# Performance work log

Hardware: AMD Instinct MI355X
Metric: run time of the kernel (lower is better)

The kernel has to match this reference:

```python
import jax, jax.numpy as jnp
import numpy as np

ROPE_BASE = 10000.0

def rope_2d(x, h, w):
    # x: (b, h, w, c); 2D RoPE, first half of pair-channels rotated by row angle, second by col angle
    b, _, _, c = x.shape
    k_max = c // 4  # c // (2 * num_spatial_dims)
    theta = 1.0 / (ROPE_BASE ** (jnp.arange(k_max, dtype=jnp.float32) / k_max))  # (k_max,)
    ang_h = jnp.arange(h, dtype=jnp.float32)[:, None] * theta  # (h, k_max)
    ang_w = jnp.arange(w, dtype=jnp.float32)[:, None] * theta  # (w, k_max)
    # angles: (h, w, 2*k_max) = cat([i*theta, j*theta], -1)
    angles = jnp.concatenate([
        jnp.broadcast_to(ang_h[:, None, :], (h, w, k_max)),
        jnp.broadcast_to(ang_w[None, :, :], (h, w, k_max)),
    ], axis=-1)
    cos = jnp.cos(angles)  # (h, w, c//2)
    sin = jnp.sin(angles)
    xr = x[..., 0::2]  # consecutive-pair real parts (b,h,w,c//2)
    xi = x[..., 1::2]
    out_r = xr * cos - xi * sin
    out_i = xr * sin + xi * cos
    return jnp.stack([out_r, out_i], axis=-1).reshape(b, h, w, c)

def linear_attention_fwd(x, h, w, qk_w, qk_b, lepe_w, lepe_b, num_heads=4):
    b, n, c = x.shape
    head_dim = c // num_heads
    qk = x @ qk_w.T + qk_b  # (b, n, 2c)
    q, k = qk[..., :c], qk[..., c:]
    v = x
    q = jax.nn.elu(q) + 1.0
    k = jax.nn.elu(k) + 1.0
    q_rope = rope_2d(q.reshape(b, h, w, c), h, w).reshape(b, n, num_heads, head_dim).transpose(0, 2, 1, 3)
    k_rope = rope_2d(k.reshape(b, h, w, c), h, w).reshape(b, n, num_heads, head_dim).transpose(0, 2, 1, 3)
    qh = q.reshape(b, n, num_heads, head_dim).transpose(0, 2, 1, 3)  # (b,H,n,d)
    kh = k.reshape(b, n, num_heads, head_dim).transpose(0, 2, 1, 3)
    vh = v.reshape(b, n, num_heads, head_dim).transpose(0, 2, 1, 3)
    k_mean = kh.mean(axis=2)  # (b,H,d)
    z = 1.0 / (jnp.einsum('bhnd,bhd->bhn', qh, k_mean) + 1e-6)  # (b,H,n)
    inv_n = 1.0 / n
    kv = jnp.einsum('bhnd,bhne->bhde', k_rope, vh) * inv_n  # (b,H,d,d)
    out = jnp.einsum('bhnd,bhde->bhne', q_rope, kv) * z[..., None]  # (b,H,n,d)
    out = out.transpose(0, 2, 1, 3).reshape(b, n, c)
    # LePE: depthwise 3x3 conv on v in NCHW
    v_img = v.reshape(b, h, w, c).transpose(0, 3, 1, 2)  # (b,c,h,w)
    lepe = jax.lax.conv_general_dilated(
        v_img, lepe_w, window_strides=(1, 1), padding='SAME',
        feature_group_count=c, dimension_numbers=('NCHW', 'OIHW', 'NCHW'))
    lepe = lepe + lepe_b[None, :, None, None]
    out = out + lepe.transpose(0, 2, 3, 1).reshape(b, n, c)
    return out.transpose(0, 2, 1).reshape(b, c, h, w)

def setup_inputs() -> dict:
    key = jax.random.key(0)
    ks = jax.random.split(key, 5)
    b, h, w, c = 16, 128, 128, 64
    n = h * w
    x = jax.random.normal(ks[0], (b, n, c), dtype=jnp.float32)
    qk_w = jax.random.normal(ks[1], (2 * c, c), dtype=jnp.float32) * (1.0 / np.sqrt(c))
    qk_b = jax.random.normal(ks[2], (2 * c,), dtype=jnp.float32) * 0.02
    lepe_w = jax.random.normal(ks[3], (c, 1, 3, 3), dtype=jnp.float32) * (1.0 / 3.0)
    lepe_b = jax.random.normal(ks[4], (c,), dtype=jnp.float32) * 0.02
    return {"x": x, "h": h, "w": w, "qk_w": qk_w, "qk_b": qk_b, "lepe_w": lepe_w, "lepe_b": lepe_b}

def reference(x, h, w, qk_w, qk_b, lepe_w, lepe_b):
    return linear_attention_fwd(x, h, w, qk_w, qk_b, lepe_w, lepe_b, num_heads=4)
```

## Files before the change

kernel.cpp:

```cpp
#include <hip/hip_runtime.h>

#define B_   16
#define C_   64
#define HH   128
#define WW   128
#define NN   (HH*WW)
#define NH   4
#define HD   16
#define PADB 72
#define PADO 66

typedef short short8 __attribute__((ext_vector_type(8)));
typedef short short4v __attribute__((ext_vector_type(4)));
typedef float f32x4  __attribute__((ext_vector_type(4)));

__device__ __forceinline__ float act_elu1(float v) {
    return v > 0.f ? v + 1.f : __expf(v);
}
__device__ __forceinline__ short f2bf(float f) {
    union { float f; unsigned u; } v; v.f = f;
    unsigned r = (v.u + 0x7FFFu + ((v.u >> 16) & 1u)) >> 16;
    return (short)r;
}

#define NEG_L2_10K_OVER16 (-0.8304820237218406f)

__global__ __launch_bounds__(256) void la_phase1(
    const float* __restrict__ x, const float* __restrict__ qk_w,
    const float* __restrict__ qk_b, float* __restrict__ g_part)
{
    __shared__ __align__(16) char pool[4*64*PADB*2 + 256*4];
    short* sW  = (short*)pool;
    short* sX  = sW  + 64*PADB;
    short* sXT = sX  + 64*PADB;
    short* sKT = sXT + 64*PADB;
    float* kmp = (float*)(sKT + 64*PADB);

    const int tid  = threadIdx.x;
    const int w    = tid >> 6;
    const int ln   = tid & 15;
    const int quad = (tid >> 4) & 3;
    const int b    = blockIdx.y;
    const int nblk = blockIdx.x;
    const float* xb = x + (size_t)b * (size_t)(NN * C_);

    #pragma unroll
    for (int it = 0; it < 4; ++it) {
        int idx = tid + 256*it;
        int row = idx & 63, k4 = (idx >> 6) << 2;
        float4 wv = *(const float4*)(qk_w + (64 + row)*64 + k4);
        short4v s4 = { f2bf(wv.x), f2bf(wv.y), f2bf(wv.z), f2bf(wv.w) };
        *(short4v*)(sW + row*PADB + k4) = s4;
    }

    float bias[4];
    #pragma unroll
    for (int nt = 0; nt < 4; ++nt) bias[nt] = qk_b[64 + 16*nt + ln];

    f32x4 acc2 = {0.f, 0.f, 0.f, 0.f};
    float kmacc[4] = {0.f, 0.f, 0.f, 0.f};

    for (int ck = 0; ck < 4; ++ck) {
        const int n0 = nblk*256 + ck*64;
        if (ck) __syncthreads();
        #pragma unroll
        for (int it = 0; it < 4; ++it) {
            int idx = tid + 256*it;
            int row = idx & 63, k4 = (idx >> 6) << 2;
            float4 xv = *(const float4*)(xb + (size_t)(n0 + row)*C_ + k4);
            short4v s4 = { f2bf(xv.x), f2bf(xv.y), f2bf(xv.z), f2bf(xv.w) };
            *(short4v*)(sX + row*PADB + k4) = s4;
            sXT[(k4+0)*PADB + row] = s4.x;
            sXT[(k4+1)*PADB + row] = s4.y;
            sXT[(k4+2)*PADB + row] = s4.z;
            sXT[(k4+3)*PADB + row] = s4.w;
        }
        __syncthreads();

        f32x4 acc[4];
        #pragma unroll
        for (int nt = 0; nt < 4; ++nt) acc[nt] = (f32x4){0.f,0.f,0.f,0.f};
        #pragma unroll
        for (int ks = 0; ks < 2; ++ks) {
            short8 a = *(const short8*)(sX + (16*w + ln)*PADB + 32*ks + 8*quad);
            #pragma unroll
            for (int nt = 0; nt < 4; ++nt) {
                short8 bf = *(const short8*)(sW + (16*nt + ln)*PADB + 32*ks + 8*quad);
                acc[nt] = __builtin_amdgcn_mfma_f32_16x16x32_bf16(a, bf, acc[nt], 0, 0, 0);
            }
        }

        #pragma unroll
        for (int nt = 0; nt < 4; ++nt) {
            const int j = 16*nt + ln;
            const int t = j >> 1;
            const float theta = exp2f(NEG_L2_10K_OVER16 * (float)(t & 15));
            const bool isY = (t < 16);
            const float sgn = (j & 1) ? 1.f : -1.f;
            #pragma unroll
            for (int r = 0; r < 4; ++r) {
                float kval = act_elu1(acc[nt][r] + bias[nt]);
                kmacc[nt] += kval;
                float P = __shfl_xor(kval, 1);
                int p_loc = 16*w + 4*quad + r;
                int n = n0 + p_loc;
                float coord = isY ? (float)(n >> 7) : (float)(n & 127);
                float s, c;
                __sincosf(coord * theta, &s, &c);
                float kr = kval*c + sgn*P*s;
                sKT[j*PADB + p_loc] = f2bf(kr);
            }
        }
        __syncthreads();

        #pragma unroll
        for (int ks = 0; ks < 2; ++ks) {
            short8 a  = *(const short8*)(sKT + (16*w + ln)*PADB + 32*ks + 8*quad);
            short8 bf = *(const short8*)(sXT + (16*w + ln)*PADB + 32*ks + 8*quad);
            acc2 = __builtin_amdgcn_mfma_f32_16x16x32_bf16(a, bf, acc2, 0, 0, 0);
        }
    }

    float* pb = g_part + (size_t)(b*64 + nblk) * 1088;
    #pragma unroll
    for (int r = 0; r < 4; ++r)
        pb[w*256 + (4*quad + r)*16 + ln] = acc2[r];

    #pragma unroll
    for (int nt = 0; nt < 4; ++nt) {
        float v = kmacc[nt];
        v += __shfl_xor(v, 16);
        v += __shfl_xor(v, 32);
        if ((tid & 63) < 16) kmp[w*64 + 16*nt + ln] = v;
    }
    __syncthreads();
    if (tid < 64)
        pb[1024 + tid] = kmp[tid] + kmp[64 + tid] + kmp[128 + tid] + kmp[192 + tid];
}

__global__ __launch_bounds__(256) void la_reduce(
    const float* __restrict__ g_part, float* __restrict__ g_kv,
    float* __restrict__ g_km)
{
    int o = blockIdx.x * 256 + threadIdx.x;
    int b = o / 1088;
    int i = o - b * 1088;
    const float* p = g_part + (size_t)(b*64) * 1088 + i;
    float s = 0.f;
    #pragma unroll 8
    for (int nb = 0; nb < 64; ++nb) s += p[(size_t)nb * 1088];
    if (i < 1024) g_kv[b*1024 + i] = s;
    else          g_km[b*64 + (i - 1024)] = s;
}

__global__ __launch_bounds__(256) void la_phase2(
    const float* __restrict__ x, const float* __restrict__ qk_w,
    const float* __restrict__ qk_b, const float* __restrict__ lepe_w,
    const float* __restrict__ lepe_b, const float* __restrict__ g_kv,
    const float* __restrict__ g_km, float* __restrict__ out)
{
    __shared__ __align__(16) char pool[32768];
    short* sX   = (short*)pool;
    short* sW   = sX + 64*PADB;
    float* sOut = (float*)pool;
    short* sQ   = (short*)(pool + 18432);
    short* sKVB = sQ + 64*PADB;

    const int tid  = threadIdx.x;
    const int w    = tid >> 6;
    const int ln   = tid & 15;
    const int quad = (tid >> 4) & 3;
    const int b    = blockIdx.y;
    const int n0   = blockIdx.x * 64;
    const float* xb = x + (size_t)b * (size_t)(NN * C_);
    const float inv_n = 1.f / (float)NN;

    #pragma unroll
    for (int it = 0; it < 4; ++it) {
        int idx = tid + 256*it;
        int row = idx & 63, k4 = (idx >> 6) << 2;
        float4 xv = *(const float4*)(xb + (size_t)(n0 + row)*C_ + k4);
        short4v s4 = { f2bf(xv.x), f2bf(xv.y), f2bf(xv.z), f2bf(xv.w) };
        *(short4v*)(sX + row*PADB + k4) = s4;
        float4 wv = *(const float4*)(qk_w + row*64 + k4);
        short4v s5 = { f2bf(wv.x), f2bf(wv.y), f2bf(wv.z), f2bf(wv.w) };
        *(short4v*)(sW + row*PADB + k4) = s5;
    }
    for (int idx = tid; idx < 1024; idx += 256) {
        int h = idx >> 8, d = (idx >> 4) & 15, e = idx & 15;
        float v = g_kv[b*1024 + idx] * inv_n;
        int rowb = h*16 + e;
        int kpos  = (h & 1) ? 16 + d : d;
        int kzero = (h & 1) ? d : 16 + d;
        sKVB[rowb*40 + kpos]  = f2bf(v);
        sKVB[rowb*40 + kzero] = 0;
    }
    float biasq[4], kmv[4];
    #pragma unroll
    for (int nt = 0; nt < 4; ++nt) {
        biasq[nt] = qk_b[16*nt + ln];
        kmv[nt]   = g_km[b*64 + 16*nt + ln];
    }
    __syncthreads();

    f32x4 acc[4];
    #pragma unroll
    for (int nt = 0; nt < 4; ++nt) acc[nt] = (f32x4){0.f,0.f,0.f,0.f};
    #pragma unroll
    for (int ks = 0; ks < 2; ++ks) {
        short8 a = *(const short8*)(sX + (16*w + ln)*PADB + 32*ks + 8*quad);
        #pragma unroll
        for (int nt = 0; nt < 4; ++nt) {
            short8 bf = *(const short8*)(sW + (16*nt + ln)*PADB + 32*ks + 8*quad);
            acc[nt] = __builtin_amdgcn_mfma_f32_16x16x32_bf16(a, bf, acc[nt], 0, 0, 0);
        }
    }

    float z_all[4][4];
    #pragma unroll
    for (int nt = 0; nt < 4; ++nt) {
        const int j = 16*nt + ln;
        const int t = j >> 1;
        const float theta = exp2f(NEG_L2_10K_OVER16 * (float)(t & 15));
        const bool isY = (t < 16);
        const float sgn = (j & 1) ? 1.f : -1.f;
        #pragma unroll
        for (int r = 0; r < 4; ++r) {
            float qval = act_elu1(acc[nt][r] + biasq[nt]);
            float dotp = qval * kmv[nt];
            dotp += __shfl_xor(dotp, 1);
            dotp += __shfl_xor(dotp, 2);
            dotp += __shfl_xor(dotp, 4);
            dotp += __shfl_xor(dotp, 8);
            z_all[nt][r] = 1.f / (dotp * inv_n + 1e-6f);
            float P = __shfl_xor(qval, 1);
            int p_loc = 16*w + 4*quad + r;
            int n = n0 + p_loc;
            float coord = isY ? (float)(n >> 7) : (float)(n & 127);
            float s, c;
            __sincosf(coord * theta, &s, &c);
            float qr = qval*c + sgn*P*s;
            sQ[p_loc*PADB + j] = f2bf(qr);
        }
    }
    __syncthreads();

    f32x4 accq[4];
    #pragma unroll
    for (int h = 0; h < 4; ++h) accq[h] = (f32x4){0.f,0.f,0.f,0.f};
    #pragma unroll
    for (int P2 = 0; P2 < 2; ++P2) {
        short8 a = *(const short8*)(sQ + (16*w + ln)*PADB + 32*P2 + 8*quad);
        #pragma unroll
        for (int hh = 0; hh < 2; ++hh) {
            int h = 2*P2 + hh;
            short8 bf = *(const short8*)(sKVB + (h*16 + ln)*40 + 8*quad);
            accq[h] = __builtin_amdgcn_mfma_f32_16x16x32_bf16(a, bf, accq[h], 0, 0, 0);
        }
    }
    #pragma unroll
    for (int h = 0; h < 4; ++h)
        #pragma unroll
        for (int r = 0; r < 4; ++r)
            sOut[(16*h + ln)*PADO + 16*w + 4*quad + r] = accq[h][r] * z_all[h][r];
    __syncthreads();

    const int ch = tid >> 2, sub = tid & 3, p0 = 16*sub;
    const int yy = n0 >> 7, xbase = n0 & 127, gx0 = xbase + p0;
    float wv9[9];
    #pragma unroll
    for (int tap = 0; tap < 9; ++tap) wv9[tap] = lepe_w[ch*9 + tap];
    const float lb = lepe_b[ch];
    float accl[16];
    #pragma unroll
    for (int j = 0; j < 16; ++j) accl[j] = 0.f;
    #pragma unroll
    for (int dy = -1; dy <= 1; ++dy) {
        int y2 = yy + dy;
        if ((unsigned)y2 >= HH) continue;
        const float* rp = xb + (size_t)(y2*WW)*C_ + ch;
        float cb[18];
        #pragma unroll
        for (int jj = 0; jj < 18; ++jj) {
            int col = gx0 - 1 + jj;
            cb[jj] = ((unsigned)col < WW) ? rp[(size_t)col*C_] : 0.f;
        }
        float w0 = wv9[(dy+1)*3 + 0], w1 = wv9[(dy+1)*3 + 1], w2 = wv9[(dy+1)*3 + 2];
        #pragma unroll
        for (int j = 0; j < 16; ++j)
            accl[j] += cb[j]*w0 + cb[j+1]*w1 + cb[j+2]*w2;
    }
    float* outp = out + (size_t)b*(size_t)(C_*NN) + (size_t)ch*NN + n0 + p0;
    #pragma unroll
    for (int g = 0; g < 4; ++g) {
        float2 a0 = *(const float2*)(sOut + ch*PADO + p0 + 4*g);
        float2 a1 = *(const float2*)(sOut + ch*PADO + p0 + 4*g + 2);
        float4 o4 = { a0.x + accl[4*g+0] + lb, a0.y + accl[4*g+1] + lb,
                      a1.x + accl[4*g+2] + lb, a1.y + accl[4*g+3] + lb };
        *(float4*)(outp + 4*g) = o4;
    }
}

extern "C" void kernel_launch(void* const* d_in, const int* in_sizes, int n_in,
                              void* d_out, int out_size, void* d_ws, size_t ws_size,
                              hipStream_t stream) {
    const float* x      = (const float*)d_in[0];
    const float* qk_w   = (const float*)d_in[3];
    const float* qk_b   = (const float*)d_in[4];
    const float* lepe_w = (const float*)d_in[5];
    const float* lepe_b = (const float*)d_in[6];
    float* out = (float*)d_out;

    float* g_part = (float*)d_ws;
    float* g_kv   = g_part + 1024*1088;
    float* g_km   = g_kv + 16*1024;

    hipLaunchKernelGGL(la_phase1, dim3(64, B_), dim3(256), 0, stream,
                       x, qk_w, qk_b, g_part);
    hipLaunchKernelGGL(la_reduce, dim3(68), dim3(256), 0, stream,
                       g_part, g_kv, g_km);
    hipLaunchKernelGGL(la_phase2, dim3(256, B_), dim3(256), 0, stream,
                       x, qk_w, qk_b, lepe_w, lepe_b, g_kv, g_km, out);
}
```

Measured before the change: 199.3 us.

## Compute Q in phase1, store bf16 Q, precompute RoPE tables and vectorize LePE

Phase1 now computes both the K and Q projections from the same x tile, writing elu(Q)+1 to a bf16 workspace buffer. Phase2 then reads this buffer directly and no longer reloads x for a second GEMM. A new init kernel precomputes the bf16 weights, a sin/cos RoPE table and transposed LePE weights, which removes per-element sincos work. The A operands are loaded straight from global memory into registers, and the depthwise conv is vectorized across 4 channels with float4 loads. In exchange it adds a 2MB-per-batch bf16 Q write and read round trip plus an extra kernel launch.

```diff
diff --git a/kernel.cpp b/kernel.cpp
--- a/kernel.cpp
+++ b/kernel.cpp
@@ -6,13 +6,13 @@
 #define WW   128
 #define NN   (HH*WW)
 #define NH   4
-#define HD   16
 #define PADB 72
 #define PADO 66
 
 typedef short short8 __attribute__((ext_vector_type(8)));
-typedef short short4v __attribute__((ext_vector_type(4)));
 typedef float f32x4  __attribute__((ext_vector_type(4)));
+
+#define NEG_L2_10K_OVER16 (-0.8304820237218406f)
 
 __device__ __forceinline__ float act_elu1(float v) {
     return v > 0.f ? v + 1.f : __expf(v);
@@ -22,19 +22,46 @@
     unsigned r = (v.u + 0x7FFFu + ((v.u >> 16) & 1u)) >> 16;
     return (short)r;
 }
-
-#define NEG_L2_10K_OVER16 (-0.8304820237218406f)
+__device__ __forceinline__ float bf2f(short s) {
+    union { unsigned u; float f; } v; v.u = ((unsigned)(unsigned short)s) << 16;
+    return v.f;
+}
+__device__ __forceinline__ unsigned cvt2bf(float lo, float hi) {
+    unsigned r;
+    asm("v_cvt_pk_bf16_f32 %0, %1, %2" : "=v"(r) : "v"(lo), "v"(hi));
+    return r;
+}
+
+__global__ __launch_bounds__(256) void la_init(
+    const float* __restrict__ qk_w, const float* __restrict__ lepe_w,
+    float2* __restrict__ g_tab, float* __restrict__ g_wT,
+    short* __restrict__ g_wbf)
+{
+    int i = blockIdx.x * 256 + threadIdx.x;
+    g_wbf[i] = f2bf(qk_w[i]);
+    if (i < 2048) {
+        int coord = i >> 4, t = i & 15;
+        float theta = exp2f(NEG_L2_10K_OVER16 * (float)t);
+        float s, c;
+        __sincosf((float)coord * theta, &s, &c);
+        g_tab[i] = make_float2(c, s);
+    }
+    if (i < 576) {
+        int tap = i >> 6, ch = i & 63;
+        g_wT[i] = lepe_w[ch * 9 + tap];
+    }
+}
 
 __global__ __launch_bounds__(256) void la_phase1(
-    const float* __restrict__ x, const float* __restrict__ qk_w,
-    const float* __restrict__ qk_b, float* __restrict__ g_part)
+    const float* __restrict__ x, const float* __restrict__ qk_b,
+    const short* __restrict__ g_wbf, const float2* __restrict__ g_tab,
+    float* __restrict__ g_part, short* __restrict__ g_q)
 {
-    __shared__ __align__(16) char pool[4*64*PADB*2 + 256*4];
-    short* sW  = (short*)pool;
-    short* sX  = sW  + 64*PADB;
-    short* sXT = sX  + 64*PADB;
+    __shared__ __align__(16) char pool[3*64*PADB*2 + 256*4];
+    short* sXT = (short*)pool;
     short* sKT = sXT + 64*PADB;
-    float* kmp = (float*)(sKT + 64*PADB);
+    short* sQ  = sKT + 64*PADB;
+    float* kmp = (float*)(sQ + 64*PADB);
 
     const int tid  = threadIdx.x;
     const int w    = tid >> 6;
@@ -44,18 +71,12 @@
     const int nblk = blockIdx.x;
     const float* xb = x + (size_t)b * (size_t)(NN * C_);
 
-    #pragma unroll
-    for (int it = 0; it < 4; ++it) {
-        int idx = tid + 256*it;
-        int row = idx & 63, k4 = (idx >> 6) << 2;
-        float4 wv = *(const float4*)(qk_w + (64 + row)*64 + k4);
-        short4v s4 = { f2bf(wv.x), f2bf(wv.y), f2bf(wv.z), f2bf(wv.w) };
-        *(short4v*)(sW + row*PADB + k4) = s4;
-    }
-
-    float bias[4];
-    #pragma unroll
-    for (int nt = 0; nt < 4; ++nt) bias[nt] = qk_b[64 + 16*nt + ln];
+    float biasK[4], biasQ[4];
+    #pragma unroll
+    for (int nt = 0; nt < 4; ++nt) {
+        biasK[nt] = qk_b[64 + 16*nt + ln];
+        biasQ[nt] = qk_b[16*nt + ln];
+    }
 
     f32x4 acc2 = {0.f, 0.f, 0.f, 0.f};
     float kmacc[4] = {0.f, 0.f, 0.f, 0.f};
@@ -68,56 +89,73 @@
             int idx = tid + 256*it;
             int row = idx & 63, k4 = (idx >> 6) << 2;
             float4 xv = *(const float4*)(xb + (size_t)(n0 + row)*C_ + k4);
-            short4v s4 = { f2bf(xv.x), f2bf(xv.y), f2bf(xv.z), f2bf(xv.w) };
-            *(short4v*)(sX + row*PADB + k4) = s4;
-            sXT[(k4+0)*PADB + row] = s4.x;
-            sXT[(k4+1)*PADB + row] = s4.y;
-            sXT[(k4+2)*PADB + row] = s4.z;
-            sXT[(k4+3)*PADB + row] = s4.w;
-        }
-        __syncthreads();
-
-        f32x4 acc[4];
-        #pragma unroll
-        for (int nt = 0; nt < 4; ++nt) acc[nt] = (f32x4){0.f,0.f,0.f,0.f};
+            unsigned p01 = cvt2bf(xv.x, xv.y), p23 = cvt2bf(xv.z, xv.w);
+            sXT[(k4+0)*PADB + row] = (short)p01;
+            sXT[(k4+1)*PADB + row] = (short)(p01 >> 16);
+            sXT[(k4+2)*PADB + row] = (short)p23;
+            sXT[(k4+3)*PADB + row] = (short)(p23 >> 16);
+        }
+        short8 aF[2];
         #pragma unroll
         for (int ks = 0; ks < 2; ++ks) {
-            short8 a = *(const short8*)(sX + (16*w + ln)*PADB + 32*ks + 8*quad);
+            const float* ap = xb + (size_t)(n0 + 16*w + ln)*C_ + 32*ks + 8*quad;
+            float4 a0 = *(const float4*)ap;
+            float4 a1 = *(const float4*)(ap + 4);
+            union { unsigned u[4]; short8 s; } af;
+            af.u[0] = cvt2bf(a0.x, a0.y);
+            af.u[1] = cvt2bf(a0.z, a0.w);
+            af.u[2] = cvt2bf(a1.x, a1.y);
+            af.u[3] = cvt2bf(a1.z, a1.w);
+            aF[ks] = af.s;
+        }
+        f32x4 ak[4], aq[4];
+        #pragma unroll
+        for (int nt = 0; nt < 4; ++nt) { ak[nt] = (f32x4){0.f,0.f,0.f,0.f}; aq[nt] = (f32x4){0.f,0.f,0.f,0.f}; }
+        #pragma unroll
+        for (int ks = 0; ks < 2; ++ks) {
             #pragma unroll
             for (int nt = 0; nt < 4; ++nt) {
-                short8 bf = *(const short8*)(sW + (16*nt + ln)*PADB + 32*ks + 8*quad);
-                acc[nt] = __builtin_amdgcn_mfma_f32_16x16x32_bf16(a, bf, acc[nt], 0, 0, 0);
+                short8 bk = *(const short8*)(g_wbf + (64 + 16*nt + ln)*C_ + 32*ks + 8*quad);
+                short8 bq = *(const short8*)(g_wbf + (16*nt + ln)*C_ + 32*ks + 8*quad);
+                ak[nt] = __builtin_amdgcn_mfma_f32_16x16x32_bf16(aF[ks], bk, ak[nt], 0, 0, 0);
+                aq[nt] = __builtin_amdgcn_mfma_f32_16x16x32_bf16(aF[ks], bq, aq[nt], 0, 0, 0);
             }
         }
-
+        const int ycoord = n0 >> 7;
+        const int x0 = n0 & 127;
         #pragma unroll
         for (int nt = 0; nt < 4; ++nt) {
             const int j = 16*nt + ln;
             const int t = j >> 1;
-            const float theta = exp2f(NEG_L2_10K_OVER16 * (float)(t & 15));
-            const bool isY = (t < 16);
             const float sgn = (j & 1) ? 1.f : -1.f;
+            float2 cs_y;
+            if (nt < 2) cs_y = g_tab[ycoord*16 + t];
             #pragma unroll
             for (int r = 0; r < 4; ++r) {
-                float kval = act_elu1(acc[nt][r] + bias[nt]);
+                int p_loc = 16*w + 4*quad + r;
+                float kval = act_elu1(ak[nt][r] + biasK[nt]);
                 kmacc[nt] += kval;
                 float P = __shfl_xor(kval, 1);
-                int p_loc = 16*w + 4*quad + r;
-                int n = n0 + p_loc;
-                float coord = isY ? (float)(n >> 7) : (float)(n & 127);
-                float s, c;
-                __sincosf(coord * theta, &s, &c);
-                float kr = kval*c + sgn*P*s;
+                float2 cs = (nt < 2) ? cs_y : g_tab[(x0 + p_loc)*16 + (t - 16)];
+                float kr = kval*cs.x + sgn*P*cs.y;
                 sKT[j*PADB + p_loc] = f2bf(kr);
+                float qval = act_elu1(aq[nt][r] + biasQ[nt]);
+                sQ[p_loc*PADB + j] = f2bf(qval);
             }
         }
         __syncthreads();
-
         #pragma unroll
         for (int ks = 0; ks < 2; ++ks) {
             short8 a  = *(const short8*)(sKT + (16*w + ln)*PADB + 32*ks + 8*quad);
             short8 bf = *(const short8*)(sXT + (16*w + ln)*PADB + 32*ks + 8*quad);
             acc2 = __builtin_amdgcn_mfma_f32_16x16x32_bf16(a, bf, acc2, 0, 0, 0);
+        }
+        #pragma unroll
+        for (int cp = 0; cp < 2; ++cp) {
+            int idx = tid + 256*cp;
+            int row = idx >> 3, c8 = idx & 7;
+            short8 qv = *(const short8*)(sQ + row*PADB + 8*c8);
+            *(short8*)(g_q + ((size_t)b*NN + n0 + row)*C_ + 8*c8) = qv;
         }
     }
 
@@ -154,17 +192,14 @@
 }
 
 __global__ __launch_bounds__(256) void la_phase2(
-    const float* __restrict__ x, const float* __restrict__ qk_w,
-    const float* __restrict__ qk_b, const float* __restrict__ lepe_w,
-    const float* __restrict__ lepe_b, const float* __restrict__ g_kv,
-    const float* __restrict__ g_km, float* __restrict__ out)
+    const float* __restrict__ x, const short* __restrict__ g_q,
+    const float* __restrict__ g_kv, const float* __restrict__ g_km,
+    const float2* __restrict__ g_tab, const float* __restrict__ g_wT,
+    const float* __restrict__ lepe_b, float* __restrict__ out)
 {
-    __shared__ __align__(16) char pool[32768];
-    short* sX   = (short*)pool;
-    short* sW   = sX + 64*PADB;
-    float* sOut = (float*)pool;
-    short* sQ   = (short*)(pool + 18432);
-    short* sKVB = sQ + 64*PADB;
+    __shared__ __align__(16) char pool[64*40*2 + 64*PADO*4];
+    short* sKVB = (short*)pool;
+    float* sOut = (float*)(pool + 64*40*2);
 
     const int tid  = threadIdx.x;
     const int w    = tid >> 6;
@@ -175,17 +210,6 @@
     const float* xb = x + (size_t)b * (size_t)(NN * C_);
     const float inv_n = 1.f / (float)NN;
 
-    #pragma unroll
-    for (int it = 0; it < 4; ++it) {
-        int idx = tid + 256*it;
-        int row = idx & 63, k4 = (idx >> 6) << 2;
-        float4 xv = *(const float4*)(xb + (size_t)(n0 + row)*C_ + k4);
-        short4v s4 = { f2bf(xv.x), f2bf(xv.y), f2bf(xv.z), f2bf(xv.w) };
-        *(short4v*)(sX + row*PADB + k4) = s4;
-        float4 wv = *(const float4*)(qk_w + row*64 + k4);
-        short4v s5 = { f2bf(wv.x), f2bf(wv.y), f2bf(wv.z), f2bf(wv.w) };
-        *(short4v*)(sW + row*PADB + k4) = s5;
-    }
     for (int idx = tid; idx < 1024; idx += 256) {
         int h = idx >> 8, d = (idx >> 4) & 15, e = idx & 15;
         float v = g_kv[b*1024 + idx] * inv_n;
@@ -195,108 +219,110 @@
         sKVB[rowb*40 + kpos]  = f2bf(v);
         sKVB[rowb*40 + kzero] = 0;
     }
-    float biasq[4], kmv[4];
-    #pragma unroll
-    for (int nt = 0; nt < 4; ++nt) {
-        biasq[nt] = qk_b[16*nt + ln];
-        kmv[nt]   = g_km[b*64 + 16*nt + ln];
-    }
+
+    const int pos    = n0 + 16*w + ln;
+    const int ycoord = n0 >> 7;
+    const int xcoord = (n0 & 127) + 16*w + ln;
+    const short* qp = g_q + ((size_t)b*NN + pos)*C_;
+    short8 q0 = *(const short8*)(qp + 8*quad);
+    short8 q1 = *(const short8*)(qp + 32 + 8*quad);
+    float qa[8], qb[8];
+    #pragma unroll
+    for (int i = 0; i < 8; ++i) { qa[i] = bf2f(q0[i]); qb[i] = bf2f(q1[i]); }
+
+    const float* kmb = g_km + b*64;
+    f32x4 km0 = *(const f32x4*)(kmb + 8*quad);
+    f32x4 km1 = *(const f32x4*)(kmb + 8*quad + 4);
+    f32x4 km2 = *(const f32x4*)(kmb + 32 + 8*quad);
+    f32x4 km3 = *(const f32x4*)(kmb + 32 + 8*quad + 4);
+    float d0 = 0.f, d1 = 0.f;
+    #pragma unroll
+    for (int i = 0; i < 4; ++i) {
+        d0 += qa[i]*km0[i] + qa[4+i]*km1[i];
+        d1 += qb[i]*km2[i] + qb[4+i]*km3[i];
+    }
+    d0 += __shfl_xor(d0, 16);
+    d1 += __shfl_xor(d1, 16);
+    const float z0 = 1.f / (d0*inv_n + 1e-6f);
+    const float z1 = 1.f / (d1*inv_n + 1e-6f);
+
+    const float* tyP = (const float*)g_tab + (ycoord*16 + 4*quad)*2;
+    const float* txP = (const float*)g_tab + (xcoord*16 + 4*quad)*2;
+    f32x4 ty0 = *(const f32x4*)tyP, ty1 = *(const f32x4*)(tyP + 4);
+    f32x4 tx0 = *(const f32x4*)txP, tx1 = *(const f32x4*)(txP + 4);
+    float cy[4] = {ty0[0], ty0[2], ty1[0], ty1[2]};
+    float sy[4] = {ty0[1], ty0[3], ty1[1], ty1[3]};
+    float cx[4] = {tx0[0], tx0[2], tx1[0], tx1[2]};
+    float sx[4] = {tx0[1], tx0[3], tx1[1], tx1[3]};
+    union { unsigned u[4]; short8 s; } A0, A1;
+    #pragma unroll
+    for (int p = 0; p < 4; ++p) {
+        float e0 = qa[2*p], o0 = qa[2*p+1];
+        A0.u[p] = cvt2bf((e0*cy[p] - o0*sy[p])*z0, (e0*sy[p] + o0*cy[p])*z0);
+        float e1 = qb[2*p], o1 = qb[2*p+1];
+        A1.u[p] = cvt2bf((e1*cx[p] - o1*sx[p])*z1, (e1*sx[p] + o1*cx[p])*z1);
+    }
+
     __syncthreads();
 
-    f32x4 acc[4];
-    #pragma unroll
-    for (int nt = 0; nt < 4; ++nt) acc[nt] = (f32x4){0.f,0.f,0.f,0.f};
-    #pragma unroll
-    for (int ks = 0; ks < 2; ++ks) {
-        short8 a = *(const short8*)(sX + (16*w + ln)*PADB + 32*ks + 8*quad);
-        #pragma unroll
-        for (int nt = 0; nt < 4; ++nt) {
-            short8 bf = *(const short8*)(sW + (16*nt + ln)*PADB + 32*ks + 8*quad);
-            acc[nt] = __builtin_amdgcn_mfma_f32_16x16x32_bf16(a, bf, acc[nt], 0, 0, 0);
-        }
-    }
-
-    float z_all[4][4];
-    #pragma unroll
-    for (int nt = 0; nt < 4; ++nt) {
-        const int j = 16*nt + ln;
-        const int t = j >> 1;
-        const float theta = exp2f(NEG_L2_10K_OVER16 * (float)(t & 15));
-        const bool isY = (t < 16);
-        const float sgn = (j & 1) ? 1.f : -1.f;
-        #pragma unroll
-        for (int r = 0; r < 4; ++r) {
-            float qval = act_elu1(acc[nt][r] + biasq[nt]);
-            float dotp = qval * kmv[nt];
-            dotp += __shfl_xor(dotp, 1);
-            dotp += __shfl_xor(dotp, 2);
-            dotp += __shfl_xor(dotp, 4);
-            dotp += __shfl_xor(dotp, 8);
-            z_all[nt][r] = 1.f / (dotp * inv_n + 1e-6f);
-            float P = __shfl_xor(qval, 1);
-            int p_loc = 16*w + 4*quad + r;
-            int n = n0 + p_loc;
-            float coord = isY ? (float)(n >> 7) : (float)(n & 127);
-            float s, c;
-            __sincosf(coord * theta, &s, &c);
-            float qr = qval*c + sgn*P*s;
-            sQ[p_loc*PADB + j] = f2bf(qr);
-        }
-    }
-    __syncthreads();
-
     f32x4 accq[4];
     #pragma unroll
     for (int h = 0; h < 4; ++h) accq[h] = (f32x4){0.f,0.f,0.f,0.f};
     #pragma unroll
-    for (int P2 = 0; P2 < 2; ++P2) {
-        short8 a = *(const short8*)(sQ + (16*w + ln)*PADB + 32*P2 + 8*quad);
-        #pragma unroll
-        for (int hh = 0; hh < 2; ++hh) {
-            int h = 2*P2 + hh;
-            short8 bf = *(const short8*)(sKVB + (h*16 + ln)*40 + 8*quad);
-            accq[h] = __builtin_amdgcn_mfma_f32_16x16x32_bf16(a, bf, accq[h], 0, 0, 0);
-        }
+    for (int hh = 0; hh < 2; ++hh) {
+        short8 bf0 = *(const short8*)(sKVB + (hh*16 + ln)*40 + 8*quad);
+        accq[hh]   = __builtin_amdgcn_mfma_f32_16x16x32_bf16(A0.s, bf0, accq[hh], 0, 0, 0);
+        short8 bf1 = *(const short8*)(sKVB + ((2+hh)*16 + ln)*40 + 8*quad);
+        accq[2+hh] = __builtin_amdgcn_mfma_f32_16x16x32_bf16(A1.s, bf1, accq[2+hh], 0, 0, 0);
     }
     #pragma unroll
     for (int h = 0; h < 4; ++h)
         #pragma unroll
         for (int r = 0; r < 4; ++r)
-            sOut[(16*h + ln)*PADO + 16*w + 4*quad + r] = accq[h][r] * z_all[h][r];
-    __syncthreads();
-
-    const int ch = tid >> 2, sub = tid & 3, p0 = 16*sub;
+            sOut[(16*h + ln)*PADO + 16*w + 4*quad + r] = accq[h][r];
+
+    const int cg = tid & 15;
+    const int pg = tid >> 4;
+    const int p0 = 4*pg;
     const int yy = n0 >> 7, xbase = n0 & 127, gx0 = xbase + p0;
-    float wv9[9];
-    #pragma unroll
-    for (int tap = 0; tap < 9; ++tap) wv9[tap] = lepe_w[ch*9 + tap];
-    const float lb = lepe_b[ch];
-    float accl[16];
-    #pragma unroll
-    for (int j = 0; j < 16; ++j) accl[j] = 0.f;
+    f32x4 accl[4];
+    #pragma unroll
+    for (int j = 0; j < 4; ++j) accl[j] = (f32x4){0.f,0.f,0.f,0.f};
     #pragma unroll
     for (int dy = -1; dy <= 1; ++dy) {
         int y2 = yy + dy;
         if ((unsigned)y2 >= HH) continue;
-        const float* rp = xb + (size_t)(y2*WW)*C_ + ch;
-        float cb[18];
-        #pragma unroll
-        for (int jj = 0; jj < 18; ++jj) {
+        f32x4 wt0 = *(const f32x4*)(g_wT + ((dy+1)*3 + 0)*C_ + 4*cg);
+        f32x4 wt1 = *(const f32x4*)(g_wT + ((dy+1)*3 + 1)*C_ + 4*cg);
+        f32x4 wt2 = *(const f32x4*)(g_wT + ((dy+1)*3 + 2)*C_ + 4*cg);
+        const float* rp = xb + (size_t)(y2*WW)*C_ + 4*cg;
+        f32x4 cb[6];
+        #pragma unroll
+        for (int jj = 0; jj < 6; ++jj) {
             int col = gx0 - 1 + jj;
-            cb[jj] = ((unsigned)col < WW) ? rp[(size_t)col*C_] : 0.f;
-        }
-        float w0 = wv9[(dy+1)*3 + 0], w1 = wv9[(dy+1)*3 + 1], w2 = wv9[(dy+1)*3 + 2];
-        #pragma unroll
-        for (int j = 0; j < 16; ++j)
-            accl[j] += cb[j]*w0 + cb[j+1]*w1 + cb[j+2]*w2;
-    }
-    float* outp = out + (size_t)b*(size_t)(C_*NN) + (size_t)ch*NN + n0 + p0;
+            cb[jj] = ((unsigned)col < WW) ? *(const f32x4*)(rp + (size_t)col*C_)
+                                          : (f32x4){0.f,0.f,0.f,0.f};
+        }
+        #pragma unroll
+        for (int j = 0; j < 4; ++j)
+            accl[j] += cb[j]*wt0 + cb[j+1]*wt1 + cb[j+2]*wt2;
+    }
+    __syncthreads();
+    #pragma unroll
+    for (int j = 0; j < 4; ++j)
+        #pragma unroll
+        for (int i = 0; i < 4; ++i)
+            sOut[(4*cg + i)*PADO + p0 + j] += accl[j][i];
+    __syncthreads();
+
+    const int ch = tid >> 2, sub = tid & 3, pp0 = 16*sub;
+    const float lb = lepe_b[ch];
+    float* outp = out + (size_t)b*(size_t)(C_*NN) + (size_t)ch*NN + n0 + pp0;
     #pragma unroll
     for (int g = 0; g < 4; ++g) {
-        float2 a0 = *(const float2*)(sOut + ch*PADO + p0 + 4*g);
-        float2 a1 = *(const float2*)(sOut + ch*PADO + p0 + 4*g + 2);
-        float4 o4 = { a0.x + accl[4*g+0] + lb, a0.y + accl[4*g+1] + lb,
-                      a1.x + accl[4*g+2] + lb, a1.y + accl[4*g+3] + lb };
+        float2 a0 = *(const float2*)(sOut + ch*PADO + pp0 + 4*g);
+        float2 a1 = *(const float2*)(sOut + ch*PADO + pp0 + 4*g + 2);
+        float4 o4 = { a0.x + lb, a0.y + lb, a1.x + lb, a1.y + lb };
         *(float4*)(outp + 4*g) = o4;
     }
 }
@@ -311,14 +337,20 @@
     const float* lepe_b = (const float*)d_in[6];
     float* out = (float*)d_out;
 
-    float* g_part = (float*)d_ws;
-    float* g_kv   = g_part + 1024*1088;
-    float* g_km   = g_kv + 16*1024;
-
-    hipLaunchKernelGGL(la_phase1, dim3(64, B_), dim3(256), 0, stream,
-                       x, qk_w, qk_b, g_part);
-    hipLaunchKernelGGL(la_reduce, dim3(68), dim3(256), 0, stream,
+    float*  g_part = (float*)d_ws;
+    float*  g_kv   = g_part + 1024*1088;
+    float*  g_km   = g_kv + 16*1024;
+    float2* g_tab  = (float2*)(g_km + 16*64);
+    float*  g_wT   = (float*)(g_tab + 2048);
+    short*  g_wbf  = (short*)(g_wT + 576);
+    short*  g_q    = (short*)(g_wbf + 8192);
+
+    hipLaunchKernelGGL(la_init,   dim3(32),      dim3(256), 0, stream,
+                       qk_w, lepe_w, g_tab, g_wT, g_wbf);
+    hipLaunchKernelGGL(la_phase1, dim3(64, B_),  dim3(256), 0, stream,
+                       x, qk_b, g_wbf, g_tab, g_part, g_q);
+    hipLaunchKernelGGL(la_reduce, dim3(68),      dim3(256), 0, stream,
                        g_part, g_kv, g_km);
     hipLaunchKernelGGL(la_phase2, dim3(256, B_), dim3(256), 0, stream,
-                       x, qk_w, qk_b, lepe_w, lepe_b, g_kv, g_km, out);
-}
+                       x, g_q, g_kv, g_km, g_tab, g_wT, lepe_b, out);
+}
```

Result: slower. 216.6 us (+8.7%).
